# Kernel optimization log

Measured on AMD Instinct MI355X. Metric: run time of the kernel, lower is better.

The kernel has to match this reference:

```python
import jax, jax.numpy as jnp
import numpy as np

CROP = 14          # initial_crop_size
POOL_K = 2         # maxpool_kernel_size == maxpool_stride


def setup_inputs() -> dict:
    key = jax.random.key(0)
    k1, k2 = jax.random.split(key)
    features = jax.random.normal(k1, (1, 50, 50, 1024), dtype=jnp.float32)
    raw = jax.random.uniform(k2, (1, 300, 4), dtype=jnp.float32)
    # well-formed normalized boxes: y1<=y2, x1<=x2
    ys = jnp.sort(raw[..., 0::2], axis=-1)
    xs = jnp.sort(raw[..., 1::2], axis=-1)
    boxes = jnp.stack([ys[..., 0], xs[..., 0], ys[..., 1], xs[..., 1]], axis=-1)
    return {"features": features, "boxes": boxes}


def _crop_and_resize(feat, boxes, crop_size):
    # feat: [H, W, C]; boxes: [N, 4] normalized (y1, x1, y2, x2)
    # Matches tf.image.crop_and_resize bilinear semantics for crop_size > 1.
    H, W, _ = feat.shape
    y1, x1, y2, x2 = boxes[:, 0], boxes[:, 1], boxes[:, 2], boxes[:, 3]
    grid = jnp.arange(crop_size, dtype=feat.dtype)  # [S]
    # sample coordinates in source pixel space: [N, S]
    ys = y1[:, None] * (H - 1) + grid[None, :] * ((y2 - y1) * (H - 1) / (crop_size - 1))[:, None]
    xs = x1[:, None] * (W - 1) + grid[None, :] * ((x2 - x1) * (W - 1) / (crop_size - 1))[:, None]
    y0f = jnp.floor(ys)
    x0f = jnp.floor(xs)
    wy = (ys - y0f)[:, :, None, None]  # [N, S, 1, 1]
    wx = (xs - x0f)[:, None, :, None]  # [N, 1, S, 1]
    y0 = jnp.clip(y0f.astype(jnp.int32), 0, H - 1)
    y1i = jnp.clip(y0 + 1, 0, H - 1)
    x0 = jnp.clip(x0f.astype(jnp.int32), 0, W - 1)
    x1i = jnp.clip(x0 + 1, 0, W - 1)
    # four corner gathers -> [N, S, S, C]
    tl = feat[y0[:, :, None], x0[:, None, :]]
    tr = feat[y0[:, :, None], x1i[:, None, :]]
    bl = feat[y1i[:, :, None], x0[:, None, :]]
    br = feat[y1i[:, :, None], x1i[:, None, :]]
    top = tl + (tr - tl) * wx
    bot = bl + (br - bl) * wx
    return top + (bot - top) * wy


def reference(features, boxes):
    # features: [1, H, W, C]; boxes: [1, N, 4]
    crops = _crop_and_resize(features[0], boxes[0], CROP)  # [N, 14, 14, C]
    N, S, _, C = crops.shape
    P = S // POOL_K
    # 2x2 stride-2 max pool (kernel == stride, S even)
    pooled = crops.reshape(N, P, POOL_K, P, POOL_K, C).max(axis=(2, 4))  # [N, 7, 7, C]
    return pooled[None]  # [1, N, 7, 7, C]
```

## Files before the change

kernel.cpp:

```cpp
#include <hip/hip_runtime.h>
#include <math.h>

#define FH 50
#define FW 50
#define FC 1024
#define FC4 256
#define NBOX 300
#define PO 7
#define CHQ 4
#define NPIX (FH * FW * FC)
#define BF16_BYTES (NPIX * 2)

typedef float nat4 __attribute__((ext_vector_type(4)));

__device__ __forceinline__ nat4 lerp4(nat4 a, nat4 b, float w) {
    return a + (b - a) * w;
}
__device__ __forceinline__ nat4 max4(nat4 a, nat4 b) {
    nat4 r;
    r.x = fmaxf(a.x, b.x);
    r.y = fmaxf(a.y, b.y);
    r.z = fmaxf(a.z, b.z);
    r.w = fmaxf(a.w, b.w);
    return r;
}
__device__ __forceinline__ nat4 bf2f(uint2 u) {
    nat4 r;
    r.x = __uint_as_float(u.x << 16);
    r.y = __uint_as_float(u.x & 0xffff0000u);
    r.z = __uint_as_float(u.y << 16);
    r.w = __uint_as_float(u.y & 0xffff0000u);
    return r;
}
__device__ __forceinline__ unsigned bfpack(float a, float b) {
    unsigned ua = __float_as_uint(a);
    unsigned ub = __float_as_uint(b);
    ua += 0x7fffu + ((ua >> 16) & 1u);
    ub += 0x7fffu + ((ub >> 16) & 1u);
    return (ua >> 16) | (ub & 0xffff0000u);
}

__global__ __launch_bounds__(256) void cvt_kernel(
    const float* __restrict__ feat, unsigned* __restrict__ ws)
{
    const int i = blockIdx.x * 256 + threadIdx.x;
    const float4 v = reinterpret_cast<const float4*>(feat)[i];
    uint2 w;
    w.x = bfpack(v.x, v.y);
    w.y = bfpack(v.z, v.w);
    reinterpret_cast<uint2*>(ws)[i] = w;
}

__global__ __launch_bounds__(64) void roi_pool_bf16_kernel(
    const unsigned* __restrict__ ws,
    const float* __restrict__ boxes,
    float* __restrict__ out)
{
    const int j = blockIdx.x & 7;
    const int k = blockIdx.x >> 3;
    const int n = j + 8 * (k / (PO * CHQ));
    if (n >= NBOX) return;
    const int r  = k % (PO * CHQ);
    const int py = r >> 2;
    const int cq = r & 3;
    const int c  = cq * 64 + threadIdx.x;

    const float by1 = boxes[n * 4 + 0];
    const float bx1 = boxes[n * 4 + 1];
    const float by2 = boxes[n * 4 + 2];
    const float bx2 = boxes[n * 4 + 3];

    const float stepy = (by2 - by1) * (49.0f / 13.0f);
    const float stepx = (bx2 - bx1) * (49.0f / 13.0f);
    const float basey = by1 * 49.0f;
    const float basex = bx1 * 49.0f;

    const float ysA = basey + (float)(2 * py) * stepy;
    const float ysB = ysA + stepy;
    const float fA = floorf(ysA); const float wyA = ysA - fA;
    const float fB = floorf(ysB); const float wyB = ysB - fB;
    const int y0A = min(max((int)fA, 0), FH - 1); const int y1A = min(y0A + 1, FH - 1);
    const int y0B = min(max((int)fB, 0), FH - 1); const int y1B = min(y0B + 1, FH - 1);

    const uint2* __restrict__ f2 = reinterpret_cast<const uint2*>(ws);
    const int r0 = y0A * FW, r1 = y1A * FW, r2 = y0B * FW, r3 = y1B * FW;

    uint2 c00, c01, c10, c11, c20, c21, c30, c31;
    uint2 n00, n01, n10, n11, n20, n21, n30, n31;

    int cc;
    {
        const float xf = floorf(basex);
        cc = min(max((int)xf, 0), FW - 1);
        const int x1 = min(cc + 1, FW - 1);
        c00 = f2[(r0 + cc) * FC4 + c];  c01 = f2[(r0 + x1) * FC4 + c];
        c10 = f2[(r1 + cc) * FC4 + c];  c11 = f2[(r1 + x1) * FC4 + c];
        c20 = f2[(r2 + cc) * FC4 + c];  c21 = f2[(r2 + x1) * FC4 + c];
        c30 = f2[(r3 + cc) * FC4 + c];  c31 = f2[(r3 + x1) * FC4 + c];
    }

    nat4 m = (nat4)(-INFINITY);
    nat4* __restrict__ obase =
        reinterpret_cast<nat4*>(out) + (size_t)(n * (PO * PO) + py * PO) * FC4 + c;

    for (int ix = 0; ix < 2 * PO; ++ix) {
        int d = 0;
        if (ix < 2 * PO - 1) {
            const float xsn = basex + (float)(ix + 1) * stepx;
            const int nx0 = min(max((int)floorf(xsn), 0), FW - 1);
            const int nx1 = min(nx0 + 1, FW - 1);
            d = nx0 - cc;
            if (d == 1) {
                n01 = f2[(r0 + nx1) * FC4 + c];
                n11 = f2[(r1 + nx1) * FC4 + c];
                n21 = f2[(r2 + nx1) * FC4 + c];
                n31 = f2[(r3 + nx1) * FC4 + c];
            } else if (d >= 2) {
                n00 = f2[(r0 + nx0) * FC4 + c];  n01 = f2[(r0 + nx1) * FC4 + c];
                n10 = f2[(r1 + nx0) * FC4 + c];  n11 = f2[(r1 + nx1) * FC4 + c];
                n20 = f2[(r2 + nx0) * FC4 + c];  n21 = f2[(r2 + nx1) * FC4 + c];
                n30 = f2[(r3 + nx0) * FC4 + c];  n31 = f2[(r3 + nx1) * FC4 + c];
            }
            cc = nx0;
        }

        {
            const float xs = basex + (float)ix * stepx;
            const float wx = xs - floorf(xs);
            const nat4 vA = lerp4(lerp4(bf2f(c00), bf2f(c01), wx),
                                  lerp4(bf2f(c10), bf2f(c11), wx), wyA);
            const nat4 vB = lerp4(lerp4(bf2f(c20), bf2f(c21), wx),
                                  lerp4(bf2f(c30), bf2f(c31), wx), wyB);
            m = max4(m, max4(vA, vB));
        }

        if (ix & 1) {
            __builtin_nontemporal_store(m, obase + (ix >> 1) * FC4);
            m = (nat4)(-INFINITY);
        }

        if (ix < 2 * PO - 1) {
            if (d == 1) {
                c00 = c01; c10 = c11; c20 = c21; c30 = c31;
                c01 = n01; c11 = n11; c21 = n21; c31 = n31;
            } else if (d >= 2) {
                c00 = n00; c01 = n01; c10 = n10; c11 = n11;
                c20 = n20; c21 = n21; c30 = n30; c31 = n31;
            }
        }
    }
}

__global__ __launch_bounds__(64) void roi_pool_f32_kernel(
    const float* __restrict__ feat,
    const float* __restrict__ boxes,
    float* __restrict__ out)
{
    const int j = blockIdx.x & 7;
    const int k = blockIdx.x >> 3;
    const int n = j + 8 * (k / (PO * CHQ));
    if (n >= NBOX) return;
    const int r  = k % (PO * CHQ);
    const int py = r >> 2;
    const int cq = r & 3;
    const int c4 = cq * 64 + threadIdx.x;

    const float by1 = boxes[n * 4 + 0];
    const float bx1 = boxes[n * 4 + 1];
    const float by2 = boxes[n * 4 + 2];
    const float bx2 = boxes[n * 4 + 3];
    const float stepy = (by2 - by1) * (49.0f / 13.0f);
    const float stepx = (bx2 - bx1) * (49.0f / 13.0f);
    const float basey = by1 * 49.0f;
    const float basex = bx1 * 49.0f;
    const float ysA = basey + (float)(2 * py) * stepy;
    const float ysB = ysA + stepy;
    const float fA = floorf(ysA); const float wyA = ysA - fA;
    const float fB = floorf(ysB); const float wyB = ysB - fB;
    const int y0A = min(max((int)fA, 0), FH - 1); const int y1A = min(y0A + 1, FH - 1);
    const int y0B = min(max((int)fB, 0), FH - 1); const int y1B = min(y0B + 1, FH - 1);

    const nat4* __restrict__ f4 = reinterpret_cast<const nat4*>(feat);
    const int rA0 = y0A * FW, rA1 = y1A * FW, rB0 = y0B * FW, rB1 = y1B * FW;

    int cc = -1000;
    nat4 A00, A01, A10, A11, B00, B01, B10, B11;
    A00 = A01 = A10 = A11 = B00 = B01 = B10 = B11 = (nat4)0.0f;
    nat4 m = (nat4)(-INFINITY);
    nat4* __restrict__ obase =
        reinterpret_cast<nat4*>(out) + (size_t)(n * (PO * PO) + py * PO) * FC4 + c4;

    for (int ix = 0; ix < 2 * PO; ++ix) {
        const float xs = basex + (float)ix * stepx;
        const float xf = floorf(xs);
        const float wx = xs - xf;
        int x0 = min(max((int)xf, 0), FW - 1);
        const int x1 = min(x0 + 1, FW - 1);
        if (x0 != cc) {
            if (x0 == cc + 1) {
                A00 = A01; A10 = A11; B00 = B01; B10 = B11;
                A01 = f4[(rA0 + x1) * FC4 + c4];
                A11 = f4[(rA1 + x1) * FC4 + c4];
                B01 = f4[(rB0 + x1) * FC4 + c4];
                B11 = f4[(rB1 + x1) * FC4 + c4];
            } else {
                A00 = f4[(rA0 + x0) * FC4 + c4];
                A01 = f4[(rA0 + x1) * FC4 + c4];
                A10 = f4[(rA1 + x0) * FC4 + c4];
                A11 = f4[(rA1 + x1) * FC4 + c4];
                B00 = f4[(rB0 + x0) * FC4 + c4];
                B01 = f4[(rB0 + x1) * FC4 + c4];
                B10 = f4[(rB1 + x0) * FC4 + c4];
                B11 = f4[(rB1 + x1) * FC4 + c4];
            }
            cc = x0;
        }
        const nat4 vA = lerp4(lerp4(A00, A01, wx), lerp4(A10, A11, wx), wyA);
        const nat4 vB = lerp4(lerp4(B00, B01, wx), lerp4(B10, B11, wx), wyB);
        m = max4(m, max4(vA, vB));
        if (ix & 1) {
            __builtin_nontemporal_store(m, obase + (ix >> 1) * FC4);
            m = (nat4)(-INFINITY);
        }
    }
}

extern "C" void kernel_launch(void* const* d_in, const int* in_sizes, int n_in,
                              void* d_out, int out_size, void* d_ws, size_t ws_size,
                              hipStream_t stream) {
    const float* feat  = (const float*)d_in[0];
    const float* boxes = (const float*)d_in[1];
    float* out = (float*)d_out;

    dim3 grid(8 * 38 * PO * CHQ);
    dim3 block(64);

    if (ws_size >= (size_t)BF16_BYTES) {
        unsigned* wsb = (unsigned*)d_ws;
        cvt_kernel<<<dim3(NPIX / 4 / 256), dim3(256), 0, stream>>>(feat, wsb);
        roi_pool_bf16_kernel<<<grid, block, 0, stream>>>(wsb, boxes, out);
    } else {
        roi_pool_f32_kernel<<<grid, block, 0, stream>>>(feat, boxes, out);
    }
}
```

Before: 100.1 us.

## Drop bf16 conversion pass and gather directly from fp32 features with prefetch

Removes the separate kernel that converted the whole feature map to bf16 in workspace, along with the bf16 gather path. The remaining kernel reads fp32 features directly and keeps the next-column software prefetch structure from the old bf16 kernel. This saves one launch and a full-map read/write pass, at the cost of doubling gather bytes per sample. It also restores exact fp32 precision.

New measurement: 107.7 us. 1.08x slower.

```diff
diff --git a/kernel.cpp b/kernel.cpp
--- a/kernel.cpp
+++ b/kernel.cpp
@@ -8,8 +8,6 @@
 #define NBOX 300
 #define PO 7
 #define CHQ 4
-#define NPIX (FH * FW * FC)
-#define BF16_BYTES (NPIX * 2)
 
 typedef float nat4 __attribute__((ext_vector_type(4)));
 
@@ -24,35 +22,9 @@
     r.w = fmaxf(a.w, b.w);
     return r;
 }
-__device__ __forceinline__ nat4 bf2f(uint2 u) {
-    nat4 r;
-    r.x = __uint_as_float(u.x << 16);
-    r.y = __uint_as_float(u.x & 0xffff0000u);
-    r.z = __uint_as_float(u.y << 16);
-    r.w = __uint_as_float(u.y & 0xffff0000u);
-    return r;
-}
-__device__ __forceinline__ unsigned bfpack(float a, float b) {
-    unsigned ua = __float_as_uint(a);
-    unsigned ub = __float_as_uint(b);
-    ua += 0x7fffu + ((ua >> 16) & 1u);
-    ub += 0x7fffu + ((ub >> 16) & 1u);
-    return (ua >> 16) | (ub & 0xffff0000u);
-}
 
-__global__ __launch_bounds__(256) void cvt_kernel(
-    const float* __restrict__ feat, unsigned* __restrict__ ws)
-{
-    const int i = blockIdx.x * 256 + threadIdx.x;
-    const float4 v = reinterpret_cast<const float4*>(feat)[i];
-    uint2 w;
-    w.x = bfpack(v.x, v.y);
-    w.y = bfpack(v.z, v.w);
-    reinterpret_cast<uint2*>(ws)[i] = w;
-}
-
-__global__ __launch_bounds__(64) void roi_pool_bf16_kernel(
-    const unsigned* __restrict__ ws,
+__global__ __launch_bounds__(64) void roi_pool_f32_kernel(
+    const float* __restrict__ feat,
     const float* __restrict__ boxes,
     float* __restrict__ out)
 {
@@ -82,21 +54,21 @@
     const int y0A = min(max((int)fA, 0), FH - 1); const int y1A = min(y0A + 1, FH - 1);
     const int y0B = min(max((int)fB, 0), FH - 1); const int y1B = min(y0B + 1, FH - 1);
 
-    const uint2* __restrict__ f2 = reinterpret_cast<const uint2*>(ws);
+    const nat4* __restrict__ f4 = reinterpret_cast<const nat4*>(feat);
     const int r0 = y0A * FW, r1 = y1A * FW, r2 = y0B * FW, r3 = y1B * FW;
 
-    uint2 c00, c01, c10, c11, c20, c21, c30, c31;
-    uint2 n00, n01, n10, n11, n20, n21, n30, n31;
+    nat4 c00, c01, c10, c11, c20, c21, c30, c31;
+    nat4 n00, n01, n10, n11, n20, n21, n30, n31;
 
     int cc;
     {
         const float xf = floorf(basex);
         cc = min(max((int)xf, 0), FW - 1);
         const int x1 = min(cc + 1, FW - 1);
-        c00 = f2[(r0 + cc) * FC4 + c];  c01 = f2[(r0 + x1) * FC4 + c];
-        c10 = f2[(r1 + cc) * FC4 + c];  c11 = f2[(r1 + x1) * FC4 + c];
-        c20 = f2[(r2 + cc) * FC4 + c];  c21 = f2[(r2 + x1) * FC4 + c];
-        c30 = f2[(r3 + cc) * FC4 + c];  c31 = f2[(r3 + x1) * FC4 + c];
+        c00 = f4[(r0 + cc) * FC4 + c];  c01 = f4[(r0 + x1) * FC4 + c];
+        c10 = f4[(r1 + cc) * FC4 + c];  c11 = f4[(r1 + x1) * FC4 + c];
+        c20 = f4[(r2 + cc) * FC4 + c];  c21 = f4[(r2 + x1) * FC4 + c];
+        c30 = f4[(r3 + cc) * FC4 + c];  c31 = f4[(r3 + x1) * FC4 + c];
     }
 
     nat4 m = (nat4)(-INFINITY);
@@ -111,15 +83,15 @@
             const int nx1 = min(nx0 + 1, FW - 1);
             d = nx0 - cc;
             if (d == 1) {
-                n01 = f2[(r0 + nx1) * FC4 + c];
-                n11 = f2[(r1 + nx1) * FC4 + c];
-                n21 = f2[(r2 + nx1) * FC4 + c];
-                n31 = f2[(r3 + nx1) * FC4 + c];
+                n01 = f4[(r0 + nx1) * FC4 + c];
+                n11 = f4[(r1 + nx1) * FC4 + c];
+                n21 = f4[(r2 + nx1) * FC4 + c];
+                n31 = f4[(r3 + nx1) * FC4 + c];
             } else if (d >= 2) {
-                n00 = f2[(r0 + nx0) * FC4 + c];  n01 = f2[(r0 + nx1) * FC4 + c];
-                n10 = f2[(r1 + nx0) * FC4 + c];  n11 = f2[(r1 + nx1) * FC4 + c];
-                n20 = f2[(r2 + nx0) * FC4 + c];  n21 = f2[(r2 + nx1) * FC4 + c];
-                n30 = f2[(r3 + nx0) * FC4 + c];  n31 = f2[(r3 + nx1) * FC4 + c];
+                n00 = f4[(r0 + nx0) * FC4 + c];  n01 = f4[(r0 + nx1) * FC4 + c];
+                n10 = f4[(r1 + nx0) * FC4 + c];  n11 = f4[(r1 + nx1) * FC4 + c];
+                n20 = f4[(r2 + nx0) * FC4 + c];  n21 = f4[(r2 + nx1) * FC4 + c];
+                n30 = f4[(r3 + nx0) * FC4 + c];  n31 = f4[(r3 + nx1) * FC4 + c];
             }
             cc = nx0;
         }
@@ -127,10 +99,8 @@
         {
             const float xs = basex + (float)ix * stepx;
             const float wx = xs - floorf(xs);
-            const nat4 vA = lerp4(lerp4(bf2f(c00), bf2f(c01), wx),
-                                  lerp4(bf2f(c10), bf2f(c11), wx), wyA);
-            const nat4 vB = lerp4(lerp4(bf2f(c20), bf2f(c21), wx),
-                                  lerp4(bf2f(c30), bf2f(c31), wx), wyB);
+            const nat4 vA = lerp4(lerp4(c00, c01, wx), lerp4(c10, c11, wx), wyA);
+            const nat4 vB = lerp4(lerp4(c20, c21, wx), lerp4(c30, c31, wx), wyB);
             m = max4(m, max4(vA, vB));
         }
 
@@ -151,95 +121,15 @@
     }
 }
 
-__global__ __launch_bounds__(64) void roi_pool_f32_kernel(
-    const float* __restrict__ feat,
-    const float* __restrict__ boxes,
-    float* __restrict__ out)
-{
-    const int j = blockIdx.x & 7;
-    const int k = blockIdx.x >> 3;
-    const int n = j + 8 * (k / (PO * CHQ));
-    if (n >= NBOX) return;
-    const int r  = k % (PO * CHQ);
-    const int py = r >> 2;
-    const int cq = r & 3;
-    const int c4 = cq * 64 + threadIdx.x;
-
-    const float by1 = boxes[n * 4 + 0];
-    const float bx1 = boxes[n * 4 + 1];
-    const float by2 = boxes[n * 4 + 2];
-    const float bx2 = boxes[n * 4 + 3];
-    const float stepy = (by2 - by1) * (49.0f / 13.0f);
-    const float stepx = (bx2 - bx1) * (49.0f / 13.0f);
-    const float basey = by1 * 49.0f;
-    const float basex = bx1 * 49.0f;
-    const float ysA = basey + (float)(2 * py) * stepy;
-    const float ysB = ysA + stepy;
-    const float fA = floorf(ysA); const float wyA = ysA - fA;
-    const float fB = floorf(ysB); const float wyB = ysB - fB;
-    const int y0A = min(max((int)fA, 0), FH - 1); const int y1A = min(y0A + 1, FH - 1);
-    const int y0B = min(max((int)fB, 0), FH - 1); const int y1B = min(y0B + 1, FH - 1);
-
-    const nat4* __restrict__ f4 = reinterpret_cast<const nat4*>(feat);
-    const int rA0 = y0A * FW, rA1 = y1A * FW, rB0 = y0B * FW, rB1 = y1B * FW;
-
-    int cc = -1000;
-    nat4 A00, A01, A10, A11, B00, B01, B10, B11;
-    A00 = A01 = A10 = A11 = B00 = B01 = B10 = B11 = (nat4)0.0f;
-    nat4 m = (nat4)(-INFINITY);
-    nat4* __restrict__ obase =
-        reinterpret_cast<nat4*>(out) + (size_t)(n * (PO * PO) + py * PO) * FC4 + c4;
-
-    for (int ix = 0; ix < 2 * PO; ++ix) {
-        const float xs = basex + (float)ix * stepx;
-        const float xf = floorf(xs);
-        const float wx = xs - xf;
-        int x0 = min(max((int)xf, 0), FW - 1);
-        const int x1 = min(x0 + 1, FW - 1);
-        if (x0 != cc) {
-            if (x0 == cc + 1) {
-                A00 = A01; A10 = A11; B00 = B01; B10 = B11;
-                A01 = f4[(rA0 + x1) * FC4 + c4];
-                A11 = f4[(rA1 + x1) * FC4 + c4];
-                B01 = f4[(rB0 + x1) * FC4 + c4];
-                B11 = f4[(rB1 + x1) * FC4 + c4];
-            } else {
-                A00 = f4[(rA0 + x0) * FC4 + c4];
-                A01 = f4[(rA0 + x1) * FC4 + c4];
-                A10 = f4[(rA1 + x0) * FC4 + c4];
-                A11 = f4[(rA1 + x1) * FC4 + c4];
-                B00 = f4[(rB0 + x0) * FC4 + c4];
-                B01 = f4[(rB0 + x1) * FC4 + c4];
-                B10 = f4[(rB1 + x0) * FC4 + c4];
-                B11 = f4[(rB1 + x1) * FC4 + c4];
-            }
-            cc = x0;
-        }
-        const nat4 vA = lerp4(lerp4(A00, A01, wx), lerp4(A10, A11, wx), wyA);
-        const nat4 vB = lerp4(lerp4(B00, B01, wx), lerp4(B10, B11, wx), wyB);
-        m = max4(m, max4(vA, vB));
-        if (ix & 1) {
-            __builtin_nontemporal_store(m, obase + (ix >> 1) * FC4);
-            m = (nat4)(-INFINITY);
-        }
-    }
-}
-
 extern "C" void kernel_launch(void* const* d_in, const int* in_sizes, int n_in,
                               void* d_out, int out_size, void* d_ws, size_t ws_size,
                               hipStream_t stream) {
+    (void)in_sizes; (void)n_in; (void)out_size; (void)d_ws; (void)ws_size;
     const float* feat  = (const float*)d_in[0];
     const float* boxes = (const float*)d_in[1];
     float* out = (float*)d_out;
 
     dim3 grid(8 * 38 * PO * CHQ);
     dim3 block(64);
-
-    if (ws_size >= (size_t)BF16_BYTES) {
-        unsigned* wsb = (unsigned*)d_ws;
-        cvt_kernel<<<dim3(NPIX / 4 / 256), dim3(256), 0, stream>>>(feat, wsb);
-        roi_pool_bf16_kernel<<<grid, block, 0, stream>>>(wsb, boxes, out);
-    } else {
-        roi_pool_f32_kernel<<<grid, block, 0, stream>>>(feat, boxes, out);
-    }
+    roi_pool_f32_kernel<<<grid, block, 0, stream>>>(feat, boxes, out);
 }
```

## Dedupe shared source rows in bf16 ROI pool and widen blocks to all channels

Applied to the files above, without the earlier changes.

The bf16 pooling kernel now checks whether the two sampled crop rows share source rows. When they do, it loads 2 or 3 distinct feature rows instead of 4, through a templated helper, which cuts gather loads and lerp work for small boxes. Blocks grow from 64 to 256 threads covering all 1024 channels, and the grid shrinks by a factor of four. The branch on row pattern is per block, so there is no divergence, but it adds code size and three template instantiations that may change register use.

Result: no change. 98.77 us (-1.4%).

```diff
diff --git a/kernel.cpp b/kernel.cpp
--- a/kernel.cpp
+++ b/kernel.cpp
@@ -51,58 +51,26 @@
     reinterpret_cast<uint2*>(ws)[i] = w;
 }
 
-__global__ __launch_bounds__(64) void roi_pool_bf16_kernel(
-    const unsigned* __restrict__ ws,
-    const float* __restrict__ boxes,
-    float* __restrict__ out)
-{
-    const int j = blockIdx.x & 7;
-    const int k = blockIdx.x >> 3;
-    const int n = j + 8 * (k / (PO * CHQ));
-    if (n >= NBOX) return;
-    const int r  = k % (PO * CHQ);
-    const int py = r >> 2;
-    const int cq = r & 3;
-    const int c  = cq * 64 + threadIdx.x;
-
-    const float by1 = boxes[n * 4 + 0];
-    const float bx1 = boxes[n * 4 + 1];
-    const float by2 = boxes[n * 4 + 2];
-    const float bx2 = boxes[n * 4 + 3];
-
-    const float stepy = (by2 - by1) * (49.0f / 13.0f);
-    const float stepx = (bx2 - bx1) * (49.0f / 13.0f);
-    const float basey = by1 * 49.0f;
-    const float basex = bx1 * 49.0f;
-
-    const float ysA = basey + (float)(2 * py) * stepy;
-    const float ysB = ysA + stepy;
-    const float fA = floorf(ysA); const float wyA = ysA - fA;
-    const float fB = floorf(ysB); const float wyB = ysB - fB;
-    const int y0A = min(max((int)fA, 0), FH - 1); const int y1A = min(y0A + 1, FH - 1);
-    const int y0B = min(max((int)fB, 0), FH - 1); const int y1B = min(y0B + 1, FH - 1);
-
-    const uint2* __restrict__ f2 = reinterpret_cast<const uint2*>(ws);
-    const int r0 = y0A * FW, r1 = y1A * FW, r2 = y0B * FW, r3 = y1B * FW;
-
-    uint2 c00, c01, c10, c11, c20, c21, c30, c31;
-    uint2 n00, n01, n10, n11, n20, n21, n30, n31;
-
+template<int NR>
+__device__ __forceinline__ void pool_rows(
+    const uint2* __restrict__ f2, const int (&rows)[NR], int c,
+    float basex, float stepx, float wyA, float wyB,
+    nat4* __restrict__ obase)
+{
+    uint2 cur[NR][2], nxt[NR][2];
     int cc;
     {
         const float xf = floorf(basex);
         cc = min(max((int)xf, 0), FW - 1);
         const int x1 = min(cc + 1, FW - 1);
-        c00 = f2[(r0 + cc) * FC4 + c];  c01 = f2[(r0 + x1) * FC4 + c];
-        c10 = f2[(r1 + cc) * FC4 + c];  c11 = f2[(r1 + x1) * FC4 + c];
-        c20 = f2[(r2 + cc) * FC4 + c];  c21 = f2[(r2 + x1) * FC4 + c];
-        c30 = f2[(r3 + cc) * FC4 + c];  c31 = f2[(r3 + x1) * FC4 + c];
+#pragma unroll
+        for (int q = 0; q < NR; ++q) {
+            cur[q][0] = f2[(rows[q] + cc) * FC4 + c];
+            cur[q][1] = f2[(rows[q] + x1) * FC4 + c];
+        }
     }
 
     nat4 m = (nat4)(-INFINITY);
-    nat4* __restrict__ obase =
-        reinterpret_cast<nat4*>(out) + (size_t)(n * (PO * PO) + py * PO) * FC4 + c;
-
     for (int ix = 0; ix < 2 * PO; ++ix) {
         int d = 0;
         if (ix < 2 * PO - 1) {
@@ -111,15 +79,15 @@
             const int nx1 = min(nx0 + 1, FW - 1);
             d = nx0 - cc;
             if (d == 1) {
-                n01 = f2[(r0 + nx1) * FC4 + c];
-                n11 = f2[(r1 + nx1) * FC4 + c];
-                n21 = f2[(r2 + nx1) * FC4 + c];
-                n31 = f2[(r3 + nx1) * FC4 + c];
+#pragma unroll
+                for (int q = 0; q < NR; ++q)
+                    nxt[q][1] = f2[(rows[q] + nx1) * FC4 + c];
             } else if (d >= 2) {
-                n00 = f2[(r0 + nx0) * FC4 + c];  n01 = f2[(r0 + nx1) * FC4 + c];
-                n10 = f2[(r1 + nx0) * FC4 + c];  n11 = f2[(r1 + nx1) * FC4 + c];
-                n20 = f2[(r2 + nx0) * FC4 + c];  n21 = f2[(r2 + nx1) * FC4 + c];
-                n30 = f2[(r3 + nx0) * FC4 + c];  n31 = f2[(r3 + nx1) * FC4 + c];
+#pragma unroll
+                for (int q = 0; q < NR; ++q) {
+                    nxt[q][0] = f2[(rows[q] + nx0) * FC4 + c];
+                    nxt[q][1] = f2[(rows[q] + nx1) * FC4 + c];
+                }
             }
             cc = nx0;
         }
@@ -127,10 +95,20 @@
         {
             const float xs = basex + (float)ix * stepx;
             const float wx = xs - floorf(xs);
-            const nat4 vA = lerp4(lerp4(bf2f(c00), bf2f(c01), wx),
-                                  lerp4(bf2f(c10), bf2f(c11), wx), wyA);
-            const nat4 vB = lerp4(lerp4(bf2f(c20), bf2f(c21), wx),
-                                  lerp4(bf2f(c30), bf2f(c31), wx), wyB);
+            const nat4 a0 = lerp4(bf2f(cur[0][0]), bf2f(cur[0][1]), wx);
+            const nat4 a1 = lerp4(bf2f(cur[1][0]), bf2f(cur[1][1]), wx);
+            const nat4 vA = lerp4(a0, a1, wyA);
+            nat4 vB;
+            if constexpr (NR == 2) {
+                vB = lerp4(a0, a1, wyB);
+            } else if constexpr (NR == 3) {
+                const nat4 a2 = lerp4(bf2f(cur[2][0]), bf2f(cur[2][1]), wx);
+                vB = lerp4(a1, a2, wyB);
+            } else {
+                const nat4 a2 = lerp4(bf2f(cur[2][0]), bf2f(cur[2][1]), wx);
+                const nat4 a3 = lerp4(bf2f(cur[3][0]), bf2f(cur[3][1]), wx);
+                vB = lerp4(a2, a3, wyB);
+            }
             m = max4(m, max4(vA, vB));
         }
 
@@ -141,13 +119,58 @@
 
         if (ix < 2 * PO - 1) {
             if (d == 1) {
-                c00 = c01; c10 = c11; c20 = c21; c30 = c31;
-                c01 = n01; c11 = n11; c21 = n21; c31 = n31;
+#pragma unroll
+                for (int q = 0; q < NR; ++q) { cur[q][0] = cur[q][1]; cur[q][1] = nxt[q][1]; }
             } else if (d >= 2) {
-                c00 = n00; c01 = n01; c10 = n10; c11 = n11;
-                c20 = n20; c21 = n21; c30 = n30; c31 = n31;
-            }
-        }
+#pragma unroll
+                for (int q = 0; q < NR; ++q) { cur[q][0] = nxt[q][0]; cur[q][1] = nxt[q][1]; }
+            }
+        }
+    }
+}
+
+__global__ __launch_bounds__(256) void roi_pool_bf16_kernel(
+    const unsigned* __restrict__ ws,
+    const float* __restrict__ boxes,
+    float* __restrict__ out)
+{
+    const int j = blockIdx.x & 7;
+    const int k = blockIdx.x >> 3;
+    const int n = j + 8 * (k / PO);
+    if (n >= NBOX) return;
+    const int py = k % PO;
+    const int c  = threadIdx.x;
+
+    const float by1 = boxes[n * 4 + 0];
+    const float bx1 = boxes[n * 4 + 1];
+    const float by2 = boxes[n * 4 + 2];
+    const float bx2 = boxes[n * 4 + 3];
+
+    const float stepy = (by2 - by1) * (49.0f / 13.0f);
+    const float stepx = (bx2 - bx1) * (49.0f / 13.0f);
+    const float basey = by1 * 49.0f;
+    const float basex = bx1 * 49.0f;
+
+    const float ysA = basey + (float)(2 * py) * stepy;
+    const float ysB = ysA + stepy;
+    const float fA = floorf(ysA); const float wyA = ysA - fA;
+    const float fB = floorf(ysB); const float wyB = ysB - fB;
+    const int y0A = min(max((int)fA, 0), FH - 1); const int y1A = min(y0A + 1, FH - 1);
+    const int y0B = min(max((int)fB, 0), FH - 1); const int y1B = min(y0B + 1, FH - 1);
+
+    const uint2* __restrict__ f2 = reinterpret_cast<const uint2*>(ws);
+    nat4* __restrict__ obase =
+        reinterpret_cast<nat4*>(out) + (size_t)(n * (PO * PO) + py * PO) * FC4 + c;
+
+    if (y0B == y0A) {
+        const int rows[2] = {y0A * FW, y1A * FW};
+        pool_rows<2>(f2, rows, c, basex, stepx, wyA, wyB, obase);
+    } else if (y0B == y1A) {
+        const int rows[3] = {y0A * FW, y1A * FW, y1B * FW};
+        pool_rows<3>(f2, rows, c, basex, stepx, wyA, wyB, obase);
+    } else {
+        const int rows[4] = {y0A * FW, y1A * FW, y0B * FW, y1B * FW};
+        pool_rows<4>(f2, rows, c, basex, stepx, wyA, wyB, obase);
     }
 }
 
@@ -228,18 +251,16 @@
 extern "C" void kernel_launch(void* const* d_in, const int* in_sizes, int n_in,
                               void* d_out, int out_size, void* d_ws, size_t ws_size,
                               hipStream_t stream) {
+    (void)in_sizes; (void)n_in; (void)out_size;
     const float* feat  = (const float*)d_in[0];
     const float* boxes = (const float*)d_in[1];
     float* out = (float*)d_out;
 
-    dim3 grid(8 * 38 * PO * CHQ);
-    dim3 block(64);
-
     if (ws_size >= (size_t)BF16_BYTES) {
         unsigned* wsb = (unsigned*)d_ws;
         cvt_kernel<<<dim3(NPIX / 4 / 256), dim3(256), 0, stream>>>(feat, wsb);
-        roi_pool_bf16_kernel<<<grid, block, 0, stream>>>(wsb, boxes, out);
+        roi_pool_bf16_kernel<<<dim3(8 * 38 * PO), dim3(256), 0, stream>>>(wsb, boxes, out);
     } else {
-        roi_pool_f32_kernel<<<grid, block, 0, stream>>>(feat, boxes, out);
-    }
-}
+        roi_pool_f32_kernel<<<dim3(8 * 38 * PO * CHQ), dim3(64), 0, stream>>>(feat, boxes, out);
+    }
+}
```
